# Kernel optimization log

Measured on AMD Instinct MI355X. Metric: run time of the kernel, lower is better.

## Reference

```python
import jax, jax.numpy as jnp
import numpy as np

NUM_CLASSES = 1000
FEAT_DIM = 256
N = 262144
ALPHA = 0.5


def setup_inputs() -> dict:
    key = jax.random.key(0)
    k1, k2, k3 = jax.random.split(key, 3)
    x = jax.random.normal(k1, (N, FEAT_DIM), dtype=jnp.float32)
    labels = jax.random.randint(k2, (N,), 0, NUM_CLASSES, dtype=jnp.int64)
    centers = jax.random.normal(k3, (NUM_CLASSES, FEAT_DIM), dtype=jnp.float32)
    return {"x": x, "labels": labels, "centers": centers}


def reference(x, labels, centers):
    # loss: mean euclidean distance to own class center, halved
    centers_batch = centers[labels]                      # [N, D] gather
    dist = jnp.sqrt(jnp.sum((x - centers_batch) ** 2, axis=1))  # [N]
    loss = dist.mean() / 2.0

    # center update (torch.no_grad block): single-pass segment mean
    C = centers.shape[0]
    sums = jax.ops.segment_sum(x, labels, num_segments=C)           # [C, D]
    counts = jax.ops.segment_sum(jnp.ones((x.shape[0],), x.dtype), labels,
                                 num_segments=C)                     # [C]
    # mean(x[mask] - center_i) = mean(x[mask]) - center_i
    mean_x = sums / jnp.maximum(counts, 1.0)[:, None]
    delta = mean_x - centers
    new_centers = jnp.where(counts[:, None] > 0,
                            centers + ALPHA * delta, centers)
    return loss, new_centers
```

## Files before the change

kernel.cpp:

```cpp
#include <hip/hip_runtime.h>
#include <math.h>


#define D 256
#define SETUP_BLOCKS 64
#define SETUP_THREADS 1024
#define U 8
#define BROWS 32

__device__ __forceinline__ void grid_barrier(int* bar) {
    __syncthreads();
    if (threadIdx.x == 0) {
        __threadfence();
        atomicAdd(bar, 1);
        while (__hip_atomic_load(bar, __ATOMIC_ACQUIRE, __HIP_MEMORY_SCOPE_AGENT)
               < SETUP_BLOCKS) {
            __builtin_amdgcn_s_sleep(2);
        }
    }
    __syncthreads();
}

__global__ __launch_bounds__(256) void init_kernel(float* __restrict__ accum,
                                                   int* __restrict__ counts,
                                                   int* __restrict__ bars,
                                                   double* __restrict__ lossacc) {
    float4* a4 = (float4*)accum;
    for (int i = blockIdx.x * 256 + threadIdx.x; i < 64000; i += gridDim.x * 256)
        a4[i] = make_float4(0.f, 0.f, 0.f, 0.f);
    if (blockIdx.x == 0) {
        for (int i = threadIdx.x; i < 1024; i += 256) counts[i] = 0;
        if (threadIdx.x < 3) bars[threadIdx.x] = 0;
        if (threadIdx.x == 0) *lossacc = 0.0;
    }
}

__global__ __launch_bounds__(SETUP_THREADS) void setup_kernel(
        const int* __restrict__ lraw, int n,
        int* __restrict__ counts, int* __restrict__ offsets,
        int* __restrict__ bar0, int* __restrict__ bar1,
        int* __restrict__ hist_all, int* __restrict__ rowidx) {
    __shared__ int sh[1024];
    __shared__ int s_flag;
    const int tid = threadIdx.x;
    const int b = blockIdx.x;

    if (tid == 0) s_flag = 0;
    sh[tid] = 0;
    __syncthreads();
    if (tid < 512 && 2 * tid + 1 < n) {
        if (lraw[2 * tid + 1]) atomicOr(&s_flag, 1);
    }
    __syncthreads();
    const int f64 = (s_flag == 0) ? 1 : 0;

    for (int i = b * SETUP_THREADS + tid; i < n; i += SETUP_BLOCKS * SETUP_THREADS) {
        const int lbl = f64 ? lraw[2 * (size_t)i] : lraw[i];
        atomicAdd(&sh[lbl], 1);
    }
    __syncthreads();
    const int myh = sh[tid];
    hist_all[b * 1024 + tid] = myh;
    if (myh) atomicAdd(&counts[tid], myh);

    grid_barrier(bar0);

    if (b == 0) {
        const int v = counts[tid];
        sh[tid] = v;
        __syncthreads();
        for (int off = 1; off < 1024; off <<= 1) {
            const int add = (tid >= off) ? sh[tid - off] : 0;
            __syncthreads();
            sh[tid] += add;
            __syncthreads();
        }
        offsets[tid] = sh[tid] - v;
    }

    grid_barrier(bar1);

    int base = offsets[tid];
    for (int pb = 0; pb < b; ++pb) base += hist_all[pb * 1024 + tid];
    __syncthreads();
    sh[tid] = base;
    __syncthreads();
    for (int i = b * SETUP_THREADS + tid; i < n; i += SETUP_BLOCKS * SETUP_THREADS) {
        const int lbl = f64 ? lraw[2 * (size_t)i] : lraw[i];
        const int pos = atomicAdd(&sh[lbl], 1);
        rowidx[pos] = i;
    }
}

__global__ __launch_bounds__(256, 4) void main_kernel(
        const float* __restrict__ x, const float* __restrict__ centers,
        const int* __restrict__ offsets, const int* __restrict__ counts,
        const int* __restrict__ rowidx,
        float* __restrict__ accum, double* __restrict__ lossacc) {
    const int c = blockIdx.x >> 1;
    const int p = blockIdx.x & 1;
    const int tid = threadIdx.x;
    const int wave = tid >> 6;
    const int lane = tid & 63;

    __shared__ int s_idx[256];
    __shared__ float s_sum[4][D];
    __shared__ float s_loss[4];

    const float4 ctr = ((const float4*)(centers + (size_t)c * D))[lane];
    const int start = offsets[c];
    const int cnt = counts[c];
    const int half = (cnt + 1) >> 1;
    const int lo = start + p * half;
    int len = cnt - p * half;
    len = len < 0 ? 0 : (len > half ? half : len);

    float4 sum = make_float4(0.f, 0.f, 0.f, 0.f);
    float lsum = 0.f;

    for (int seg0 = 0; seg0 < len; seg0 += 256) {
        const int seg = min(256, len - seg0);
        __syncthreads();
        if (tid < seg) s_idx[tid] = rowidx[lo + seg0 + tid];
        __syncthreads();

        const int nb = (seg + BROWS - 1) / BROWS;

        float4 A[U], B[U];

        auto LOADB = [&](int bb, float4* buf) {
            #pragma unroll
            for (int k = 0; k < U; ++k) {
                const int pos = bb * BROWS + wave * U + k;
                const int safe = (pos < seg) ? pos : 0;
                const int r = s_idx[safe];
                buf[k] = ((const float4*)(x + (size_t)r * D))[lane];
            }
        };
        auto PROCB = [&](int bb, const float4* buf) {
            #pragma unroll
            for (int k = 0; k < U; ++k) {
                const int pos = bb * BROWS + wave * U + k;
                const float w = (pos < seg) ? 1.f : 0.f;
                const float4 v = buf[k];
                sum.x = fmaf(w, v.x, sum.x);
                sum.y = fmaf(w, v.y, sum.y);
                sum.z = fmaf(w, v.z, sum.z);
                sum.w = fmaf(w, v.w, sum.w);
                const float dx = v.x - ctr.x, dy = v.y - ctr.y;
                const float dz = v.z - ctr.z, dw = v.w - ctr.w;
                float sq = w * (dx * dx + dy * dy + dz * dz + dw * dw);
                #pragma unroll
                for (int o = 32; o; o >>= 1) sq += __shfl_xor(sq, o, 64);
                lsum += sqrtf(sq);
            }
        };

        LOADB(0, A);
        for (int bb = 0; bb < nb; bb += 2) {
            LOADB(bb + 1, B);
            PROCB(bb, A);
            LOADB(bb + 2, A);
            PROCB(bb + 1, B);
        }
    }

    ((float4*)&s_sum[wave][lane * 4])[0] = sum;
    if (lane == 0) s_loss[wave] = lsum;
    __syncthreads();

    const float tot = s_sum[0][tid] + s_sum[1][tid] + s_sum[2][tid] + s_sum[3][tid];
    atomicAdd(&accum[(size_t)c * D + tid], tot);
    if (tid == 0) {
        const double bl = (double)(s_loss[0] + s_loss[1] + s_loss[2] + s_loss[3]);
        atomicAdd(lossacc, bl);
    }
}

__global__ __launch_bounds__(256) void finalize_kernel(
        const float* __restrict__ accum, const float* __restrict__ centers,
        const int* __restrict__ counts, const double* __restrict__ lossacc,
        int n, float* __restrict__ out) {
    const int c = blockIdx.x;
    const int t = threadIdx.x;
    const int cnt = counts[c];
    const float cs = centers[(size_t)c * D + t];
    const float s = accum[(size_t)c * D + t];
    const float o = (cnt > 0) ? cs + 0.5f * (s / (float)cnt - cs) : cs;
    out[1 + (size_t)c * D + t] = o;
    if (c == 0 && t == 0) out[0] = (float)(*lossacc / (double)n * 0.5);
}

extern "C" void kernel_launch(void* const* d_in, const int* in_sizes, int n_in,
                              void* d_out, int out_size, void* d_ws, size_t ws_size,
                              hipStream_t stream) {
    const float* x       = (const float*)d_in[0];
    const int*   lraw    = (const int*)d_in[1];
    const float* centers = (const float*)d_in[2];
    float* out = (float*)d_out;

    const int n = in_sizes[1];
    const int C = in_sizes[2] / D;

    char* ws = (char*)d_ws;
    int*    counts   = (int*)(ws + 0);
    int*    offsets  = (int*)(ws + 4096);
    int*    bars     = (int*)(ws + 8192);
    double* lossacc  = (double*)(ws + 8208);
    int*    hist_all = (int*)(ws + 16384);
    int*    rowidx   = (int*)(ws + 524288);
    float*  accum    = (float*)(ws + 2097152);

    hipLaunchKernelGGL(init_kernel, dim3(128), dim3(256), 0, stream,
                       accum, counts, bars, lossacc);
    hipLaunchKernelGGL(setup_kernel, dim3(SETUP_BLOCKS), dim3(SETUP_THREADS), 0, stream,
                       lraw, n, counts, offsets, &bars[0], &bars[1], hist_all, rowidx);
    hipLaunchKernelGGL(main_kernel, dim3(C * 2), dim3(256), 0, stream,
                       x, centers, offsets, counts, rowidx, accum, lossacc);
    hipLaunchKernelGGL(finalize_kernel, dim3(C), dim3(256), 0, stream,
                       accum, centers, counts, lossacc, n, out);
}
```

Baseline: 403.0 us.

## Stream gathered rows into an LDS ring via async global_load_lds

Replaces the register double-buffered gather of x rows with asynchronous global-to-LDS loads into a per-wave ring of 10 slots. Each wave keeps 8 row loads in flight and throttles with explicit s_waitcnt vmcnt before consuming each row from LDS. The aim is to hide gather latency without tying up vector registers for staging. The cost is about 40KB of shared memory per block, which may limit occupancy, and the scheme depends on hand-counted vmcnt waits being correct.

```diff
diff --git a/kernel.cpp b/kernel.cpp
--- a/kernel.cpp
+++ b/kernel.cpp
@@ -5,8 +5,11 @@
 #define D 256
 #define SETUP_BLOCKS 64
 #define SETUP_THREADS 1024
-#define U 8
-#define BROWS 32
+#define CH 256
+#define SLOTS 10
+#define INFLIGHT 8
+
+#define VMWAIT(n) asm volatile("s_waitcnt vmcnt(" #n ")" ::: "memory")
 
 __device__ __forceinline__ void grid_barrier(int* bar) {
     __syncthreads();
@@ -103,7 +106,8 @@
     const int wave = tid >> 6;
     const int lane = tid & 63;
 
-    __shared__ int s_idx[256];
+    __shared__ int   s_idx[CH];
+    __shared__ float s_stage[4][SLOTS][D];
     __shared__ float s_sum[4][D];
     __shared__ float s_loss[4];
 
@@ -118,51 +122,60 @@
     float4 sum = make_float4(0.f, 0.f, 0.f, 0.f);
     float lsum = 0.f;
 
-    for (int seg0 = 0; seg0 < len; seg0 += 256) {
-        const int seg = min(256, len - seg0);
+    float* const st = &s_stage[wave][0][0];
+
+    for (int cb = 0; cb < len; cb += CH) {
+        const int seg = min(CH, len - cb);
         __syncthreads();
-        if (tid < seg) s_idx[tid] = rowidx[lo + seg0 + tid];
+        if (tid < seg) s_idx[tid] = rowidx[lo + cb + tid];
         __syncthreads();
 
-        const int nb = (seg + BROWS - 1) / BROWS;
-
-        float4 A[U], B[U];
-
-        auto LOADB = [&](int bb, float4* buf) {
+        const int jtot = (seg + 3) >> 2;
+
+        auto ISSUE = [&](int j) {
+            const int pos  = wave + 4 * j;
+            const int safe = (pos < seg) ? pos : (seg - 1);
+            const int r    = s_idx[safe];
+            const float* src = x + (size_t)r * D + lane * 4;
+            float* dst = st + (j % SLOTS) * D;
+            __builtin_amdgcn_global_load_lds(
+                (const __attribute__((address_space(1))) void*)src,
+                (__attribute__((address_space(3))) void*)dst, 16, 0, 0);
+        };
+        auto PROCR = [&](int j) {
+            const int jj  = (j < 0) ? 0 : j;
+            const int pos = wave + 4 * jj;
+            const float w = (j >= 0 && pos < seg) ? 1.f : 0.f;
+            const float4 v = ((const float4*)(st + (jj % SLOTS) * D))[lane];
+            sum.x = fmaf(w, v.x, sum.x);
+            sum.y = fmaf(w, v.y, sum.y);
+            sum.z = fmaf(w, v.z, sum.z);
+            sum.w = fmaf(w, v.w, sum.w);
+            const float dx = v.x - ctr.x, dy = v.y - ctr.y;
+            const float dz = v.z - ctr.z, dw = v.w - ctr.w;
+            float sq = w * (dx * dx + dy * dy + dz * dz + dw * dw);
             #pragma unroll
-            for (int k = 0; k < U; ++k) {
-                const int pos = bb * BROWS + wave * U + k;
-                const int safe = (pos < seg) ? pos : 0;
-                const int r = s_idx[safe];
-                buf[k] = ((const float4*)(x + (size_t)r * D))[lane];
-            }
+            for (int o = 32; o; o >>= 1) sq += __shfl_xor(sq, o, 64);
+            lsum += sqrtf(sq);
         };
-        auto PROCB = [&](int bb, const float4* buf) {
-            #pragma unroll
-            for (int k = 0; k < U; ++k) {
-                const int pos = bb * BROWS + wave * U + k;
-                const float w = (pos < seg) ? 1.f : 0.f;
-                const float4 v = buf[k];
-                sum.x = fmaf(w, v.x, sum.x);
-                sum.y = fmaf(w, v.y, sum.y);
-                sum.z = fmaf(w, v.z, sum.z);
-                sum.w = fmaf(w, v.w, sum.w);
-                const float dx = v.x - ctr.x, dy = v.y - ctr.y;
-                const float dz = v.z - ctr.z, dw = v.w - ctr.w;
-                float sq = w * (dx * dx + dy * dy + dz * dz + dw * dw);
-                #pragma unroll
-                for (int o = 32; o; o >>= 1) sq += __shfl_xor(sq, o, 64);
-                lsum += sqrtf(sq);
-            }
-        };
-
-        LOADB(0, A);
-        for (int bb = 0; bb < nb; bb += 2) {
-            LOADB(bb + 1, B);
-            PROCB(bb, A);
-            LOADB(bb + 2, A);
-            PROCB(bb + 1, B);
+
+        #pragma unroll
+        for (int j = 0; j < INFLIGHT; ++j)
+            ISSUE(j < jtot ? j : jtot - 1);
+
+        for (int j = INFLIGHT; j < jtot; ++j) {
+            VMWAIT(7);
+            PROCR(j - INFLIGHT);
+            ISSUE(j);
         }
+        VMWAIT(7); PROCR(jtot - 8);
+        VMWAIT(6); PROCR(jtot - 7);
+        VMWAIT(5); PROCR(jtot - 6);
+        VMWAIT(4); PROCR(jtot - 5);
+        VMWAIT(3); PROCR(jtot - 4);
+        VMWAIT(2); PROCR(jtot - 3);
+        VMWAIT(1); PROCR(jtot - 2);
+        VMWAIT(0); PROCR(jtot - 1);
     }
 
     ((float4*)&s_sum[wave][lane * 4])[0] = sum;
```

Measured after the change: 402.2 us. Within noise of the previous version (-0.2%).
